# Optimization experiments

Hardware: AMD Instinct MI355X
Metric: run time of the kernel (lower is better)

The kernel has to match this reference:

```python
import jax, jax.numpy as jnp
import numpy as np

IN_CH = 2
K = 5
STRIDE = 1
NQ = IN_CH * K          # n_qubits = kernel_size * in_channels
DIM = 2 ** NQ           # quantum state dimension = 1024


def setup_inputs() -> dict:
    key = jax.random.key(0)
    k1, k2, k3 = jax.random.split(key, 3)
    x = jax.random.normal(k1, (16, IN_CH, 4096), dtype=jnp.float32)
    entangle_matrix = jax.random.normal(k2, (DIM, DIM), dtype=jnp.float32) / np.sqrt(DIM).astype(np.float32)
    theta = jax.random.uniform(k3, (NQ,), dtype=jnp.float32, minval=0.0, maxval=2.0 * np.pi)
    return {"x": x, "entangle_matrix": entangle_matrix, "theta": theta}


def _im2col(x):
    # torch: unfold(-1,K,stride) -> (B,C,nW,K); cat over channel dim along -1 -> (B,nW,C*K)
    B, C, L = x.shape
    nW = (L - K) // STRIDE + 1
    idx = jnp.arange(nW)[:, None] * STRIDE + jnp.arange(K)[None, :]   # (nW, K)
    cols = x[:, :, idx]                                               # (B, C, nW, K)
    cols = jnp.transpose(cols, (0, 2, 1, 3)).reshape(B * nW, C * K)   # channel-major last dim
    return cols, nW


def reference(x, entangle_matrix, theta):
    cols, nW = _im2col(x)           # (N, NQ) rotation angles, one per qubit
    N = cols.shape[0]
    # --- RY(x_i) angle encoding from |0...0>: product state of [cos(x/2), sin(x/2)] ---
    half = 0.5 * cols
    c, s = jnp.cos(half), jnp.sin(half)          # (N, NQ)
    state = jnp.ones((N, 1), dtype=x.dtype)
    for i in range(NQ):                          # loop over fixed small n_qubits
        qi = jnp.stack([c[:, i], s[:, i]], axis=-1)            # (N, 2)
        state = (state[:, :, None] * qi[:, None, :]).reshape(N, -1)
    # --- entangling layer: psi' = E @ psi (the custom kernel matmul) ---
    state = state @ entangle_matrix.T            # (N, DIM)
    # --- trainable per-qubit RY(theta_i) layer ---
    ct, st = jnp.cos(0.5 * theta), jnp.sin(0.5 * theta)
    for i in range(NQ):
        s4 = state.reshape(N, 2 ** i, 2, 2 ** (NQ - 1 - i))
        a0, a1 = s4[:, :, 0], s4[:, :, 1]
        state = jnp.stack([ct[i] * a0 - st[i] * a1,
                           st[i] * a0 + ct[i] * a1], axis=2).reshape(N, DIM)
    # --- measure <Z> on qubit 0 (most significant bit) ---
    p = (state * state).reshape(N, 2, DIM // 2)
    z = p[:, 0].sum(-1) - p[:, 1].sum(-1)        # (N,)
    B = x.shape[0]
    return z.reshape(B, 1, -1, nW)
```

## Files before the change

### kernel.cpp

```cpp
#include <hip/hip_runtime.h>
#include <math.h>

#define B_SZ   16
#define L_SZ   4096
#define NWIN   4092
#define U3     243
#define UPAD   256

#define APK_OFF 0
#define M_OFF   65536
#define EXTRA_OFF (M_OFF + 1048576)

typedef __attribute__((ext_vector_type(8))) __bf16 bf16x8;
typedef __attribute__((ext_vector_type(4))) float f32x4;

__device__ __forceinline__ float sel3(int t, float c, float s) {
    return t == 0 ? 1.0f : (t == 1 ? c : s);
}

__device__ __forceinline__ int apk_idx(int u, int v) {
    return (((u >> 4) * 8 + (v >> 5)) * 64 + ((u & 15) | (((v >> 3) & 3) << 4))) * 8 + (v & 7);
}

__device__ __forceinline__ void bfsplit(float x, float& hf, float& lf) {
    hf = __uint_as_float(__float_as_uint(x) & 0xFFFF0000u);
    lf = x - hf;
}

__global__ __launch_bounds__(256, 4) void mgemm_ker(const float* __restrict__ E,
                                                    const float* __restrict__ theta,
                                                    float* __restrict__ M,
                                                    float* __restrict__ Mp_extra) {
    __shared__ float SA[32][72];
    __shared__ float SB[32][72];
    __shared__ uint4 AfH[4 * 64], AfL[4 * 64];
    __shared__ uint4 BfH[4 * 64], BfL[4 * 64];

    int t = blockIdx.x;
    int bj = 0;
    while (t >= 16 - bj) { t -= 16 - bj; ++bj; }
    int bk = bj + t;
    int ks = blockIdx.z;
    int tid = threadIdx.x;
    int lane = tid & 63;
    int wave = tid >> 6;

    float th = theta[0];
    float st, ct;
    __sincosf(th, &st, &ct);

    f32x4 acc[4];
    #pragma unroll
    for (int kt = 0; kt < 4; ++kt) acc[kt] = (f32x4){0.f, 0.f, 0.f, 0.f};

    int kchunk = 1024 / gridDim.z;
    int k0 = ks * kchunk;
    int lr = tid >> 3;
    int lcq = (tid & 7) * 8;

    for (int d0 = k0; d0 < k0 + kchunk; d0 += 32) {
        bool hi = d0 >= 512;
        int dp = hi ? (d0 - 512) : (d0 + 512);
        float4 a0 = *(const float4*)&E[(d0 + lr) * 1024 + bj * 64 + lcq];
        float4 a1 = *(const float4*)&E[(d0 + lr) * 1024 + bj * 64 + lcq + 4];
        float4 q0 = *(const float4*)&E[(d0 + lr) * 1024 + bk * 64 + lcq];
        float4 q1 = *(const float4*)&E[(d0 + lr) * 1024 + bk * 64 + lcq + 4];
        float4 p0 = *(const float4*)&E[(dp + lr) * 1024 + bk * 64 + lcq];
        float4 p1 = *(const float4*)&E[(dp + lr) * 1024 + bk * 64 + lcq + 4];
        float4 y0, y1;
        if (!hi) {
            y0.x = ct * q0.x - st * p0.x; y0.y = ct * q0.y - st * p0.y;
            y0.z = ct * q0.z - st * p0.z; y0.w = ct * q0.w - st * p0.w;
            y1.x = ct * q1.x - st * p1.x; y1.y = ct * q1.y - st * p1.y;
            y1.z = ct * q1.z - st * p1.z; y1.w = ct * q1.w - st * p1.w;
        } else {
            y0.x = -st * p0.x - ct * q0.x; y0.y = -st * p0.y - ct * q0.y;
            y0.z = -st * p0.z - ct * q0.z; y0.w = -st * p0.w - ct * q0.w;
            y1.x = -st * p1.x - ct * q1.x; y1.y = -st * p1.y - ct * q1.y;
            y1.z = -st * p1.z - ct * q1.z; y1.w = -st * p1.w - ct * q1.w;
        }
        __syncthreads();
        *(float4*)&SA[lr][lcq] = a0;
        *(float4*)&SA[lr][lcq + 4] = a1;
        *(float4*)&SB[lr][lcq] = y0;
        *(float4*)&SB[lr][lcq + 4] = y1;
        __syncthreads();

        {
            unsigned ahw[4], alw[4], bhw[4], blw[4];
            float pah, pal, pbh, pbl;
            #pragma unroll
            for (int i = 0; i < 8; ++i) {
                float av = SA[wave * 8 + i][lane];
                float bv = SB[wave * 8 + i][lane];
                float ah, al, bh, bl;
                bfsplit(av, ah, al);
                bfsplit(bv, bh, bl);
                if (i & 1) {
                    ahw[i >> 1] = __byte_perm(__float_as_uint(pah), __float_as_uint(ah), 0x7632);
                    alw[i >> 1] = __byte_perm(__float_as_uint(pal), __float_as_uint(al), 0x7632);
                    bhw[i >> 1] = __byte_perm(__float_as_uint(pbh), __float_as_uint(bh), 0x7632);
                    blw[i >> 1] = __byte_perm(__float_as_uint(pbl), __float_as_uint(bl), 0x7632);
                } else { pah = ah; pal = al; pbh = bh; pbl = bl; }
            }
            int slot = ((lane >> 4) << 6) + (lane & 15) + (wave << 4);
            AfH[slot] = make_uint4(ahw[0], ahw[1], ahw[2], ahw[3]);
            AfL[slot] = make_uint4(alw[0], alw[1], alw[2], alw[3]);
            BfH[slot] = make_uint4(bhw[0], bhw[1], bhw[2], bhw[3]);
            BfL[slot] = make_uint4(blw[0], blw[1], blw[2], blw[3]);
        }
        __syncthreads();

        uint4 ahu = AfH[wave * 64 + lane];
        uint4 alu = AfL[wave * 64 + lane];
        bf16x8 ah = __builtin_bit_cast(bf16x8, ahu);
        bf16x8 al = __builtin_bit_cast(bf16x8, alu);
        #pragma unroll
        for (int kt = 0; kt < 4; ++kt) {
            uint4 bhu = BfH[kt * 64 + lane];
            uint4 blu = BfL[kt * 64 + lane];
            bf16x8 bh = __builtin_bit_cast(bf16x8, bhu);
            bf16x8 bl = __builtin_bit_cast(bf16x8, blu);
            acc[kt] = __builtin_amdgcn_mfma_f32_16x16x32_bf16(ah, bh, acc[kt], 0, 0, 0);
            acc[kt] = __builtin_amdgcn_mfma_f32_16x16x32_bf16(ah, bl, acc[kt], 0, 0, 0);
            acc[kt] = __builtin_amdgcn_mfma_f32_16x16x32_bf16(al, bh, acc[kt], 0, 0, 0);
        }
    }

    float* dst = (ks == 0) ? M : (Mp_extra + (ks - 1) * 1048576);
    #pragma unroll
    for (int kt = 0; kt < 4; ++kt) {
        #pragma unroll
        for (int i = 0; i < 4; ++i) {
            int r = bj * 64 + wave * 16 + ((lane >> 4) << 2) + i;
            int c = bk * 64 + kt * 16 + (lane & 15);
            dst[((r >> 5) * 32 + (c >> 5)) * 1024 + (r & 31) * 32 + (c & 31)] = acc[kt][i];
        }
    }
}

__global__ __launch_bounds__(256) void cwht_ker(const float* __restrict__ M,
                                                const float* __restrict__ Mp_extra,
                                                int S,
                                                unsigned short* __restrict__ ApkH) {
    __shared__ float D[1024];
    int mx = blockIdx.x;
    int mxh = mx >> 5, mxl = mx & 31;
    int tid = threadIdx.x;
    float v[4];
    #pragma unroll
    for (int k = 0; k < 4; ++k) {
        int j = tid + k * 256;
        int jh = j >> 5, jl = j & 31;
        int kh = jh ^ mxh, kl = jl ^ mxl;
        int off;
        if ((jh >> 1) <= (kh >> 1)) off = ((jh * 32 + kh) * 32 + jl) * 32 + kl;
        else                        off = ((kh * 32 + jh) * 32 + kl) * 32 + jl;
        float t = M[off];
        for (int s = 1; s < S; ++s) t += Mp_extra[(s - 1) * 1048576 + off];
        v[k] = t;
    }
    #pragma unroll
    for (int s = 0; s < 6; ++s) {
        int bit = (tid >> s) & 1;
        #pragma unroll
        for (int k = 0; k < 4; ++k) {
            float p = __shfl_xor(v[k], 1 << s, 64);
            v[k] = bit ? (p - v[k]) : (v[k] + p);
        }
    }
    #pragma unroll
    for (int k = 0; k < 4; ++k) D[tid + k * 256] = v[k];
    __syncthreads();
    {
        int b6 = (tid >> 6) & 1, b7 = (tid >> 7) & 1;
        #pragma unroll
        for (int k = 0; k < 4; ++k) {
            float p64  = D[(tid ^ 64)  + k * 256];
            float p128 = D[(tid ^ 128) + k * 256];
            float p192 = D[(tid ^ 192) + k * 256];
            float ta = b6 ? (p64 - v[k])   : (v[k] + p64);
            float tb = b6 ? (p192 - p128)  : (p128 + p192);
            v[k] = b7 ? (tb - ta) : (ta + tb);
        }
    }
    {
        float a0 = v[0] + v[1], a1 = v[0] - v[1], a2 = v[2] + v[3], a3 = v[2] - v[3];
        v[0] = a0 + a2; v[1] = a1 + a3; v[2] = a0 - a2; v[3] = a1 - a3;
    }
    #pragma unroll
    for (int k = 0; k < 4; ++k) {
        int mz = tid + k * 256;
        if (mz & mx) continue;
        int u = 0, vv = 0;
        #pragma unroll
        for (int i = 0; i < 5; ++i) {
            int bit = 9 - i;
            int tt = ((mx >> bit) & 1) ? 2 : (((mz >> bit) & 1) ? 1 : 0);
            u = u * 3 + tt;
        }
        #pragma unroll
        for (int i = 5; i < 10; ++i) {
            int bit = 9 - i;
            int tt = ((mx >> bit) & 1) ? 2 : (((mz >> bit) & 1) ? 1 : 0);
            vv = vv * 3 + tt;
        }
        float val = v[k] * (1.0f / 1024.0f);
        unsigned hh = __float_as_uint(val) & 0xFFFF0000u;
        float lf = val - __uint_as_float(hh);
        unsigned ll = __float_as_uint(lf) >> 16;
        int idx = apk_idx(u, vv);
        ApkH[idx] = (unsigned short)(hh >> 16);
        ApkH[idx + 65536] = (unsigned short)ll;
    }
    if (mx == 0) {
        for (int e = tid; e < 13 * 256; e += 256) {
            int u = 243 + (e >> 8), vv = e & 255;
            int idx = apk_idx(u, vv);
            ApkH[idx] = 0; ApkH[idx + 65536] = 0;
        }
        for (int e = tid; e < 243 * 13; e += 256) {
            int u = e / 13, vv = 243 + (e - (e / 13) * 13);
            int idx = apk_idx(u, vv);
            ApkH[idx] = 0; ApkH[idx + 65536] = 0;
        }
    }
}

__global__ __launch_bounds__(256, 3) void main_ker(const float* __restrict__ x,
                                                   const uint4* __restrict__ Apk,
                                                   float* __restrict__ out) {
    __shared__ float trg[4][68];
    __shared__ __align__(16) unsigned char arena[33280];
    unsigned short* F1h = (unsigned short*)arena;
    unsigned short* F1l = (unsigned short*)(arena + 16640);
    float* F0 = (float*)arena;
    __shared__ float red[16][16];

    int tid = threadIdx.x;
    int w0 = blockIdx.x * 64;
    int b  = blockIdx.y;
    int lane = tid & 63;
    int wave = tid >> 6;
    int wb = tid & 63;
    int wu = __builtin_amdgcn_readfirstlane(wave);

    for (int p = tid; p < 68; p += 256) {
        int pos = w0 + p;
        bool ok = pos < L_SZ;
        float x1 = ok ? x[b * 8192 + 4096 + pos] : 0.f;
        float x0 = ok ? x[b * 8192 + pos] : 0.f;
        float c1v, s1v, c0v, s0v;
        __sincosf(x1, &s1v, &c1v);
        __sincosf(x0, &s0v, &c0v);
        if (!ok) { c1v = 0.f; s1v = 0.f; c0v = 0.f; s0v = 0.f; }
        trg[0][p] = c1v; trg[1][p] = s1v; trg[2][p] = c0v; trg[3][p] = s0v;
    }

    f32x4 acc[4][4];
    #pragma unroll
    for (int ut = 0; ut < 4; ++ut)
        #pragma unroll
        for (int wt = 0; wt < 4; ++wt)
            acc[ut][wt] = (f32x4){0.f, 0.f, 0.f, 0.f};

    __syncthreads();

    float c1r[5], s1r[5];
    #pragma unroll
    for (int k = 0; k < 5; ++k) { c1r[k] = trg[0][wb + k]; s1r[k] = trg[1][wb + k]; }

    const uint4* Ahi = Apk;
    const uint4* Alo = Apk + 8192;

    #pragma unroll 1
    for (int h = 0; h < 2; ++h) {
        if (h) __syncthreads();
        {
            int gv = h * 128 + wu * 32;
            int t0 = gv / 81; int rr = gv - t0 * 81;
            int t1 = rr / 27; rr -= t1 * 27;
            int t2 = rr / 9;  rr -= t2 * 9;
            int t3 = rr / 3;  int t4 = rr - t3 * 3;
            float g0 = sel3(t0, c1r[0], s1r[0]);
            float g1 = sel3(t1, c1r[1], s1r[1]);
            float g2 = sel3(t2, c1r[2], s1r[2]);
            float g3 = sel3(t3, c1r[3], s1r[3]);
            float p0123 = g0 * g1 * g2 * g3;
            #pragma unroll
            for (int p8 = 0; p8 < 4; ++p8) {
                unsigned hw[4], lw[4];
                float prevh, prevl;
                #pragma unroll
                for (int i = 0; i < 8; ++i) {
                    float val = p0123 * sel3(t4, c1r[4], s1r[4]);
                    float hf, lf;
                    bfsplit(val, hf, lf);
                    if (i & 1) {
                        hw[i >> 1] = __byte_perm(__float_as_uint(prevh), __float_as_uint(hf), 0x7632);
                        lw[i >> 1] = __byte_perm(__float_as_uint(prevl), __float_as_uint(lf), 0x7632);
                    } else { prevh = hf; prevl = lf; }
                    if (++t4 == 3) { t4 = 0;
                        if (++t3 == 3) { t3 = 0;
                            if (++t2 == 3) { t2 = 0;
                                if (++t1 == 3) { t1 = 0; ++t0; g0 = sel3(t0, c1r[0], s1r[0]); }
                                g1 = sel3(t1, c1r[1], s1r[1]);
                            }
                            g2 = sel3(t2, c1r[2], s1r[2]);
                        }
                        g3 = sel3(t3, c1r[3], s1r[3]);
                        p0123 = g0 * g1 * g2 * g3;
                    }
                }
                int vp = wu * 4 + p8;
                *(uint4*)&F1h[(vp * 65 + wb) * 8] = make_uint4(hw[0], hw[1], hw[2], hw[3]);
                *(uint4*)&F1l[(vp * 65 + wb) * 8] = make_uint4(lw[0], lw[1], lw[2], lw[3]);
            }
        }
        __syncthreads();

        #pragma unroll
        for (int kl = 0; kl < 4; ++kl) {
            int ks = h * 4 + kl;
            uint4 a_h[4], a_l[4];
            #pragma unroll
            for (int ut = 0; ut < 4; ++ut) {
                int idx = ((wave * 4 + ut) * 8 + ks) * 64 + lane;
                a_h[ut] = Ahi[idx];
                a_l[ut] = Alo[idx];
            }
            int vp = kl * 4 + (lane >> 4);
            #pragma unroll
            for (int wt = 0; wt < 4; ++wt) {
                int off = (vp * 65 + wt * 16 + (lane & 15)) * 8;
                uint4 b_h = *(const uint4*)&F1h[off];
                uint4 b_l = *(const uint4*)&F1l[off];
                bf16x8 bh = __builtin_bit_cast(bf16x8, b_h);
                bf16x8 bl = __builtin_bit_cast(bf16x8, b_l);
                #pragma unroll
                for (int ut = 0; ut < 4; ++ut) {
                    bf16x8 ah = __builtin_bit_cast(bf16x8, a_h[ut]);
                    bf16x8 al = __builtin_bit_cast(bf16x8, a_l[ut]);
                    acc[ut][wt] = __builtin_amdgcn_mfma_f32_16x16x32_bf16(ah, bh, acc[ut][wt], 0, 0, 0);
                    acc[ut][wt] = __builtin_amdgcn_mfma_f32_16x16x32_bf16(ah, bl, acc[ut][wt], 0, 0, 0);
                    acc[ut][wt] = __builtin_amdgcn_mfma_f32_16x16x32_bf16(al, bh, acc[ut][wt], 0, 0, 0);
                }
            }
        }
    }

    int c = lane & 15;
    float c0b[5], s0b[5];
    #pragma unroll
    for (int k = 0; k < 5; ++k) { c0b[k] = trg[2][wb + k]; s0b[k] = trg[3][wb + k]; }
    float zcol[4] = {0.f, 0.f, 0.f, 0.f};

    __syncthreads();
    #pragma unroll 1
    for (int hp = 0; hp < 2; ++hp) {
        if (hp) __syncthreads();
        {
            int gu = hp * 128 + wu * 32;
            int t0 = gu / 81; int rr = gu - t0 * 81;
            int t1 = rr / 27; rr -= t1 * 27;
            int t2 = rr / 9;  rr -= t2 * 9;
            int t3 = rr / 3;  int t4 = rr - t3 * 3;
            float g0 = sel3(t0, c0b[0], s0b[0]);
            float g1 = sel3(t1, c0b[1], s0b[1]);
            float g2 = sel3(t2, c0b[2], s0b[2]);
            float g3 = sel3(t3, c0b[3], s0b[3]);
            float p0123 = g0 * g1 * g2 * g3;
            #pragma unroll
            for (int s = 0; s < 32; ++s) {
                float val = p0123 * sel3(t4, c0b[4], s0b[4]);
                F0[(wu * 32 + s) * 65 + wb] = val;
                if (++t4 == 3) { t4 = 0;
                    if (++t3 == 3) { t3 = 0;
                        if (++t2 == 3) { t2 = 0;
                            if (++t1 == 3) { t1 = 0; ++t0; g0 = sel3(t0, c0b[0], s0b[0]); }
                            g1 = sel3(t1, c0b[1], s0b[1]);
                        }
                        g2 = sel3(t2, c0b[2], s0b[2]);
                    }
                    g3 = sel3(t3, c0b[3], s0b[3]);
                    p0123 = g0 * g1 * g2 * g3;
                }
            }
        }
        __syncthreads();
        if ((wave >> 1) == hp) {
            int wloc = wave & 1;
            int qb = (lane >> 4) << 2;
            #pragma unroll
            for (int ut = 0; ut < 4; ++ut) {
                #pragma unroll
                for (int r = 0; r < 4; ++r) {
                    int uloc = wloc * 64 + ut * 16 + qb + r;
                    #pragma unroll
                    for (int wt = 0; wt < 4; ++wt)
                        zcol[wt] += F0[uloc * 65 + wt * 16 + c] * acc[ut][wt][r];
                }
            }
        }
    }

    #pragma unroll
    for (int wt = 0; wt < 4; ++wt) {
        float v = zcol[wt];
        v += __shfl_xor(v, 16, 64);
        v += __shfl_xor(v, 32, 64);
        if ((lane >> 4) == 0) red[wave * 4 + wt][lane] = v;
    }
    __syncthreads();
    if (tid < 64) {
        int wt = tid >> 4, cc = tid & 15;
        float z = red[0 * 4 + wt][cc] + red[1 * 4 + wt][cc]
                + red[2 * 4 + wt][cc] + red[3 * 4 + wt][cc];
        int w = wt * 16 + cc;
        if (w0 + w < NWIN) out[b * NWIN + w0 + w] = z;
    }
}

extern "C" void kernel_launch(void* const* d_in, const int* in_sizes, int n_in,
                              void* d_out, int out_size, void* d_ws, size_t ws_size,
                              hipStream_t stream) {
    const float* x     = (const float*)d_in[0];
    const float* E     = (const float*)d_in[1];
    const float* theta = (const float*)d_in[2];
    float* out = (float*)d_out;
    float* ws = (float*)d_ws;

    uint4* Apk = (uint4*)(ws + APK_OFF);
    float* M   = ws + M_OFF;
    float* Mx  = ws + EXTRA_OFF;

    size_t need2 = (size_t)(EXTRA_OFF + 1 * 1048576) * 4;
    int S = (ws_size >= need2) ? 2 : 1;

    mgemm_ker<<<dim3(136, 1, S), 256, 0, stream>>>(E, theta, M, Mx);
    cwht_ker<<<1024, 256, 0, stream>>>(M, Mx, S, (unsigned short*)Apk);
    main_ker<<<dim3(64, 16), 256, 0, stream>>>(x, Apk, out);
}
```

Before: 75.43 us.

## Split-K sum kernel, 4-way split, A-fragment prefetch, lower occupancy bound

Raises the split-K factor for the precompute GEMM to 4 when the workspace allows it. A separate vectorized sum kernel reduces the partial products, so the WHT kernel no longer gathers scattered partials. In the main kernel, global A-fragment loads are double-buffered one k-step ahead to hide load latency. The launch bound drops from 3 to 2 blocks per SM to free registers for the prefetch, at the cost of lower occupancy and one extra kernel launch.

```diff
diff --git a/kernel.cpp b/kernel.cpp
--- a/kernel.cpp
+++ b/kernel.cpp
@@ -139,9 +139,19 @@
     }
 }
 
+__global__ __launch_bounds__(256) void sum_ker(float* __restrict__ M,
+                                               const float* __restrict__ Mp_extra,
+                                               int S) {
+    int i = blockIdx.x * 256 + threadIdx.x;
+    float4 v = ((const float4*)M)[i];
+    for (int s = 1; s < S; ++s) {
+        float4 p = ((const float4*)(Mp_extra + (s - 1) * 1048576))[i];
+        v.x += p.x; v.y += p.y; v.z += p.z; v.w += p.w;
+    }
+    ((float4*)M)[i] = v;
+}
+
 __global__ __launch_bounds__(256) void cwht_ker(const float* __restrict__ M,
-                                                const float* __restrict__ Mp_extra,
-                                                int S,
                                                 unsigned short* __restrict__ ApkH) {
     __shared__ float D[1024];
     int mx = blockIdx.x;
@@ -156,9 +166,7 @@
         int off;
         if ((jh >> 1) <= (kh >> 1)) off = ((jh * 32 + kh) * 32 + jl) * 32 + kl;
         else                        off = ((kh * 32 + jh) * 32 + kl) * 32 + jl;
-        float t = M[off];
-        for (int s = 1; s < S; ++s) t += Mp_extra[(s - 1) * 1048576 + off];
-        v[k] = t;
+        v[k] = M[off];
     }
     #pragma unroll
     for (int s = 0; s < 6; ++s) {
@@ -227,7 +235,7 @@
     }
 }
 
-__global__ __launch_bounds__(256, 3) void main_ker(const float* __restrict__ x,
+__global__ __launch_bounds__(256, 2) void main_ker(const float* __restrict__ x,
                                                    const uint4* __restrict__ Apk,
                                                    float* __restrict__ out) {
     __shared__ float trg[4][68];
@@ -272,6 +280,14 @@
 
     const uint4* Ahi = Apk;
     const uint4* Alo = Apk + 8192;
+
+    uint4 a_h[4], a_l[4];
+    #pragma unroll
+    for (int ut = 0; ut < 4; ++ut) {
+        int idx = ((wave * 4 + ut) * 8 + 0) * 64 + lane;
+        a_h[ut] = Ahi[idx];
+        a_l[ut] = Alo[idx];
+    }
 
     #pragma unroll 1
     for (int h = 0; h < 2; ++h) {
@@ -322,12 +338,14 @@
         #pragma unroll
         for (int kl = 0; kl < 4; ++kl) {
             int ks = h * 4 + kl;
-            uint4 a_h[4], a_l[4];
-            #pragma unroll
-            for (int ut = 0; ut < 4; ++ut) {
-                int idx = ((wave * 4 + ut) * 8 + ks) * 64 + lane;
-                a_h[ut] = Ahi[idx];
-                a_l[ut] = Alo[idx];
+            uint4 na_h[4], na_l[4];
+            if (ks < 7) {
+                #pragma unroll
+                for (int ut = 0; ut < 4; ++ut) {
+                    int idx = ((wave * 4 + ut) * 8 + ks + 1) * 64 + lane;
+                    na_h[ut] = Ahi[idx];
+                    na_l[ut] = Alo[idx];
+                }
             }
             int vp = kl * 4 + (lane >> 4);
             #pragma unroll
@@ -345,6 +363,10 @@
                     acc[ut][wt] = __builtin_amdgcn_mfma_f32_16x16x32_bf16(ah, bl, acc[ut][wt], 0, 0, 0);
                     acc[ut][wt] = __builtin_amdgcn_mfma_f32_16x16x32_bf16(al, bh, acc[ut][wt], 0, 0, 0);
                 }
+            }
+            if (ks < 7) {
+                #pragma unroll
+                for (int ut = 0; ut < 4; ++ut) { a_h[ut] = na_h[ut]; a_l[ut] = na_l[ut]; }
             }
         }
     }
@@ -434,10 +456,12 @@
     float* M   = ws + M_OFF;
     float* Mx  = ws + EXTRA_OFF;
 
+    size_t need4 = (size_t)(EXTRA_OFF + 3 * 1048576) * 4;
     size_t need2 = (size_t)(EXTRA_OFF + 1 * 1048576) * 4;
-    int S = (ws_size >= need2) ? 2 : 1;
+    int S = (ws_size >= need4) ? 4 : ((ws_size >= need2) ? 2 : 1);
 
     mgemm_ker<<<dim3(136, 1, S), 256, 0, stream>>>(E, theta, M, Mx);
-    cwht_ker<<<1024, 256, 0, stream>>>(M, Mx, S, (unsigned short*)Apk);
+    if (S > 1) sum_ker<<<1024, 256, 0, stream>>>(M, Mx, S);
+    cwht_ker<<<1024, 256, 0, stream>>>(M, (unsigned short*)Apk);
     main_ker<<<dim3(64, 16), 256, 0, stream>>>(x, Apk, out);
 }
```

Measured after the change: 70.62 us. 1.07x faster.
